# Optimization experiments

Hardware: AMD Instinct MI355X
Metric: run time of the kernel (lower is better)

The kernel has to match this reference:

```python
import jax, jax.numpy as jnp
import numpy as np

N = 50000        # nodes
E = 800000       # edges (avg degree 16)
F = 64           # in/out feature dim (scatter into zeros_like(x) forces out==in)
H = 128          # hidden dim
CIN = 2 * F + 1  # combined_features dim


def setup_inputs() -> dict:
    key = jax.random.key(0)
    ks = jax.random.split(key, 12)
    x = jax.random.normal(ks[0], (N, F), dtype=jnp.float32)
    pos = jax.random.normal(ks[1], (N, 3), dtype=jnp.float32)
    edge_index = jax.random.randint(ks[2], (2, E), 0, N, dtype=jnp.int64)
    s1 = 1.0 / np.sqrt(CIN)
    s2 = 1.0 / np.sqrt(H)
    W1x = jax.random.uniform(ks[3], (CIN, H), jnp.float32, -s1, s1)
    b1x = jax.random.uniform(ks[4], (H,), jnp.float32, -s1, s1)
    W2x = jax.random.uniform(ks[5], (H, F), jnp.float32, -s2, s2)
    b2x = jax.random.uniform(ks[6], (F,), jnp.float32, -s2, s2)
    W1p = jax.random.uniform(ks[7], (CIN, H), jnp.float32, -s1, s1)
    b1p = jax.random.uniform(ks[8], (H,), jnp.float32, -s1, s1)
    W2p = jax.random.uniform(ks[9], (H, 1), jnp.float32, -s2, s2)
    b2p = jax.random.uniform(ks[10], (1,), jnp.float32, -s2, s2)
    return {"x": x, "pos": pos, "edge_index": edge_index,
            "W1x": W1x, "b1x": b1x, "W2x": W2x, "b2x": b2x,
            "W1p": W1p, "b1p": b1p, "W2p": W2p, "b2p": b2p}


def reference(x, pos, edge_index, W1x, b1x, W2x, b2x, W1p, b1p, W2p, b2p):
    row, col = edge_index[0], edge_index[1]
    rel_pos = pos[row] - pos[col]                              # [E, 3]
    dist_sq = jnp.sum(rel_pos * rel_pos, axis=-1, keepdims=True)  # [E, 1]
    combined = jnp.concatenate([x[row], x[col], dist_sq], axis=-1)  # [E, 2F+1]
    # phi_x: Linear -> SiLU -> Linear
    msg_x = jax.nn.silu(combined @ W1x + b1x) @ W2x + b2x      # [E, F]
    aggregated_x = jax.ops.segment_sum(msg_x, col, num_segments=x.shape[0])
    # phi_pos: Linear -> SiLU -> Linear (scalar weight per edge)
    weight_pos = jax.nn.silu(combined @ W1p + b1p) @ W2p + b2p  # [E, 1]
    pos_update = weight_pos * rel_pos                           # [E, 3]
    aggregated_pos = jax.ops.segment_sum(pos_update, col, num_segments=pos.shape[0])
    return aggregated_x, aggregated_pos
```

## Files before the change

### kernel.cpp

```cpp
#include <hip/hip_runtime.h>

typedef short short8 __attribute__((ext_vector_type(8)));
typedef float floatx4 __attribute__((ext_vector_type(4)));

__device__ __forceinline__ unsigned short f2bf(float f) {
  unsigned int u = __float_as_uint(f);
  u += 0x7FFFu + ((u >> 16) & 1u);
  return (unsigned short)(u >> 16);
}

#if __has_builtin(__builtin_amdgcn_cvt_pk_bf16_f32)
typedef __bf16 bf16x2_t __attribute__((ext_vector_type(2)));
__device__ __forceinline__ unsigned int pk2bf(float lo, float hi) {
  bf16x2_t v = __builtin_amdgcn_cvt_pk_bf16_f32(lo, hi);
  return __builtin_bit_cast(unsigned int, v);
}
#else
__device__ __forceinline__ unsigned int pk2bf(float lo, float hi) {
  return (unsigned)f2bf(lo) | ((unsigned)f2bf(hi) << 16);
}
#endif

__global__ void k_xcvt(const float* __restrict__ x, unsigned short* __restrict__ xb, int n) {
  int i = (blockIdx.x * 256 + threadIdx.x) * 8;
  if (i < n) {
    float4 a = *(const float4*)(x + i);
    float4 b = *(const float4*)(x + i + 4);
    uint4 o;
    o.x = pk2bf(a.x, a.y); o.y = pk2bf(a.z, a.w);
    o.z = pk2bf(b.x, b.y); o.w = pk2bf(b.z, b.w);
    *(uint4*)(xb + i) = o;
  }
}

__global__ void prep_weights(const float* __restrict__ W1x, const float* __restrict__ W1p,
                             const float* __restrict__ b1x, const float* __restrict__ b1p,
                             const float* __restrict__ W2x, unsigned short* __restrict__ wbuf) {
  int i = blockIdx.x * 256 + threadIdx.x;
  if (i >= 49152) return;
  float v;
  if (i < 40960) {
    const float* W = (i < 20480) ? W1x : W1p;
    const float* B = (i < 20480) ? b1x : b1p;
    int j = (i < 20480) ? i : i - 20480;
    int jj   = j & 7;
    int lane = (j >> 3) & 63;
    int ks   = (j >> 9) % 5;
    int nt   = j / 2560;
    int k = ks*32 + (lane >> 4)*8 + jj;
    int n = nt*16 + (lane & 15);
    v = (k < 129) ? W[k*128 + n] : (k == 129 ? B[n] : 0.0f);
  } else {
    int j = i - 40960;
    int jj   = j & 7;
    int lane = (j >> 3) & 63;
    int ks   = (j >> 9) & 3;
    int nt   = j >> 11;
    int k = ks*32 + (lane >> 4)*8 + jj;
    int n = nt*16 + (lane & 15);
    v = W2x[k*64 + n];
  }
  wbuf[i] = f2bf(v);
}

__global__ void k_hist(const int* __restrict__ col, int E, int* __restrict__ hist) {
  int i = blockIdx.x * 256 + threadIdx.x;
  if (i < E) atomicAdd(&hist[col[i]], 1);
}

__global__ __launch_bounds__(256) void k_scan_a(const int* __restrict__ hist, int N,
                                                int* __restrict__ excl, int* __restrict__ bsum) {
  __shared__ int wtot[4], wexc[4];
  int t = threadIdx.x, lane = t & 63, w = t >> 6;
  int base = blockIdx.x * 1024 + t * 4;
  int v0 = (base + 0 < N) ? hist[base + 0] : 0;
  int v1 = (base + 1 < N) ? hist[base + 1] : 0;
  int v2 = (base + 2 < N) ? hist[base + 2] : 0;
  int v3 = (base + 3 < N) ? hist[base + 3] : 0;
  int T = v0 + v1 + v2 + v3;
  int inc = T;
  #pragma unroll
  for (int s = 1; s < 64; s <<= 1) {
    int u = __shfl_up(inc, s, 64);
    if (lane >= s) inc += u;
  }
  if (lane == 63) wtot[w] = inc;
  __syncthreads();
  if (t == 0) {
    int a = 0;
    #pragma unroll
    for (int i = 0; i < 4; ++i) { wexc[i] = a; a += wtot[i]; }
    bsum[blockIdx.x] = a;
  }
  __syncthreads();
  int tex = wexc[w] + (inc - T);
  if (base + 0 < N) excl[base + 0] = tex;
  if (base + 1 < N) excl[base + 1] = tex + v0;
  if (base + 2 < N) excl[base + 2] = tex + v0 + v1;
  if (base + 3 < N) excl[base + 3] = tex + v0 + v1 + v2;
}

__global__ void k_scan_b(const int* __restrict__ bsum, int* __restrict__ boff, int NB) {
  int lane = threadIdx.x;
  int v = (lane < NB) ? bsum[lane] : 0;
  int inc = v;
  #pragma unroll
  for (int s = 1; s < 64; s <<= 1) {
    int u = __shfl_up(inc, s, 64);
    if (lane >= s) inc += u;
  }
  if (lane < NB) boff[lane] = inc - v;
}

__global__ void k_scatter(const int* __restrict__ row, const int* __restrict__ col, int E,
                          int* __restrict__ excl, const int* __restrict__ boff,
                          int2* __restrict__ sedge) {
  int i = blockIdx.x * 256 + threadIdx.x;
  if (i < E) {
    int c = col[i];
    int p = atomicAdd(&excl[c], 1) + boff[c >> 10];
    sedge[p] = make_int2(row[i], c);
  }
}

__global__ __launch_bounds__(256) void mp_main(
    const float* __restrict__ x, const unsigned short* __restrict__ xb, int use_xb,
    const float* __restrict__ pos,
    const int2* __restrict__ sedge,
    const int* __restrict__ rowp, const int* __restrict__ colp,
    int E, int sorted,
    const float* __restrict__ b2x, const float* __restrict__ W2p,
    const float* __restrict__ b2p,
    const unsigned short* __restrict__ wbuf,
    float* __restrict__ out_x, float* __restrict__ out_pos)
{
  __shared__ __align__(16) unsigned short C_lds[64][168];
  __shared__ __align__(16) unsigned short H_lds[64][136];
  __shared__ float rel_lds[64][3];
  __shared__ int   col_sh[64];
  __shared__ float wsum[4][64];

  const int t    = threadIdx.x;
  const int e0   = blockIdx.x * 64;
  const int wv   = t >> 6;
  const int lane = t & 63;
  const int quad = lane >> 4;
  const int lc   = lane & 15;

  if (t < 64) {
    int e = e0 + t;
    float rp0 = 0.f, rp1 = 0.f, rp2 = 0.f, dsq = 0.f; int c = -1;
    if (e < E) {
      int r;
      if (sorted) { int2 rc = sedge[e]; r = rc.x; c = rc.y; }
      else        { r = rowp[e]; c = colp[e]; }
      float pr0 = pos[r*3+0], pr1 = pos[r*3+1], pr2 = pos[r*3+2];
      float pc0 = pos[c*3+0], pc1 = pos[c*3+1], pc2 = pos[c*3+2];
      rp0 = pr0 - pc0; rp1 = pr1 - pc1; rp2 = pr2 - pc2;
      dsq = rp0*rp0 + rp1*rp1 + rp2*rp2;
    }
    rel_lds[t][0] = rp0; rel_lds[t][1] = rp1; rel_lds[t][2] = rp2;
    col_sh[t] = c;
    C_lds[t][128] = f2bf(dsq);
    C_lds[t][129] = 0x3F80;
    #pragma unroll
    for (int k = 130; k < 160; ++k) C_lds[t][k] = 0;
  }
  {
    const int s = t >> 2, p = t & 3;
    const int e = e0 + s;
    uint4 r0, r1, c0, c1;
    if (e < E) {
      int r, c;
      if (sorted) { int2 rc = sedge[e]; r = rc.x; c = rc.y; }
      else        { r = rowp[e]; c = colp[e]; }
      if (use_xb) {
        const uint4* xr = (const uint4*)(xb + (size_t)r*64 + p*16);
        const uint4* xc = (const uint4*)(xb + (size_t)c*64 + p*16);
        r0 = xr[0]; r1 = xr[1];
        c0 = xc[0]; c1 = xc[1];
      } else {
        const float4* xr = (const float4*)(x + (size_t)r*64 + p*16);
        const float4* xc = (const float4*)(x + (size_t)c*64 + p*16);
        float4 a0 = xr[0], a1 = xr[1], a2 = xr[2], a3 = xr[3];
        float4 d0 = xc[0], d1 = xc[1], d2 = xc[2], d3 = xc[3];
        r0 = make_uint4(pk2bf(a0.x,a0.y), pk2bf(a0.z,a0.w), pk2bf(a1.x,a1.y), pk2bf(a1.z,a1.w));
        r1 = make_uint4(pk2bf(a2.x,a2.y), pk2bf(a2.z,a2.w), pk2bf(a3.x,a3.y), pk2bf(a3.z,a3.w));
        c0 = make_uint4(pk2bf(d0.x,d0.y), pk2bf(d0.z,d0.w), pk2bf(d1.x,d1.y), pk2bf(d1.z,d1.w));
        c1 = make_uint4(pk2bf(d2.x,d2.y), pk2bf(d2.z,d2.w), pk2bf(d3.x,d3.y), pk2bf(d3.z,d3.w));
      }
    } else {
      r0 = r1 = c0 = c1 = make_uint4(0u, 0u, 0u, 0u);
    }
    uint4* dr = (uint4*)&C_lds[s][p*16];
    dr[0] = r0; dr[1] = r1;
    uint4* dc = (uint4*)&C_lds[s][64 + p*16];
    dc[0] = c0; dc[1] = c1;
  }
  __syncthreads();

  const short8* __restrict__ w1x_f = (const short8*)(wbuf);
  const short8* __restrict__ w1p_f = (const short8*)(wbuf + 20480);
  const short8* __restrict__ w2x_f = (const short8*)(wbuf + 40960);

  short8 a1x[2][5], a1p[2][5], a2w[4];
  #pragma unroll
  for (int i = 0; i < 2; ++i) {
    int hti = wv + 4*i;
    #pragma unroll
    for (int ks = 0; ks < 5; ++ks) {
      a1x[i][ks] = w1x_f[(hti*5 + ks)*64 + lane];
      a1p[i][ks] = w1p_f[(hti*5 + ks)*64 + lane];
    }
  }
  #pragma unroll
  for (int ks = 0; ks < 4; ++ks) a2w[ks] = w2x_f[(wv*4 + ks)*64 + lane];

  float wp2[2][4], b2xr[4];
  #pragma unroll
  for (int i = 0; i < 2; ++i)
    #pragma unroll
    for (int r = 0; r < 4; ++r) wp2[i][r] = W2p[(wv + 4*i)*16 + quad*4 + r];
  #pragma unroll
  for (int r = 0; r < 4; ++r) b2xr[r] = b2x[wv*16 + quad*4 + r];
  const float b2ps = b2p[0];

  #pragma unroll 2
  for (int et = 0; et < 4; ++et) {
    floatx4 ax0 = {0,0,0,0}, ax1 = {0,0,0,0}, ap0 = {0,0,0,0}, ap1 = {0,0,0,0};
    #pragma unroll
    for (int ks = 0; ks < 5; ++ks) {
      short8 b = *(const short8*)&C_lds[et*16 + lc][ks*32 + quad*8];
      ax0 = __builtin_amdgcn_mfma_f32_16x16x32_bf16(a1x[0][ks], b, ax0, 0, 0, 0);
      ax1 = __builtin_amdgcn_mfma_f32_16x16x32_bf16(a1x[1][ks], b, ax1, 0, 0, 0);
      ap0 = __builtin_amdgcn_mfma_f32_16x16x32_bf16(a1p[0][ks], b, ap0, 0, 0, 0);
      ap1 = __builtin_amdgcn_mfma_f32_16x16x32_bf16(a1p[1][ks], b, ap1, 0, 0, 0);
    }
    float ps = 0.f;
    #pragma unroll
    for (int i = 0; i < 2; ++i) {
      floatx4 axx = i ? ax1 : ax0;
      floatx4 app = i ? ap1 : ap0;
      float sx[4];
      #pragma unroll
      for (int r = 0; r < 4; ++r) {
        float h  = axx[r];
        sx[r] = h * __builtin_amdgcn_rcpf(1.f + __expf(-h));
        float hp = app[r];
        float sp = hp * __builtin_amdgcn_rcpf(1.f + __expf(-hp));
        ps += sp * wp2[i][r];
      }
      *(uint2*)&H_lds[et*16 + lc][(wv + 4*i)*16 + quad*4] =
          make_uint2(pk2bf(sx[0], sx[1]), pk2bf(sx[2], sx[3]));
    }
    ps += __shfl_xor(ps, 16, 64);
    ps += __shfl_xor(ps, 32, 64);
    if (lane < 16) wsum[wv][et*16 + lane] = ps;
  }
  __syncthreads();

  #pragma unroll 2
  for (int et = 0; et < 4; ++et) {
    floatx4 acc = {0,0,0,0};
    #pragma unroll
    for (int ks = 0; ks < 4; ++ks) {
      short8 b = *(const short8*)&H_lds[et*16 + lc][ks*32 + quad*8];
      acc = __builtin_amdgcn_mfma_f32_16x16x32_bf16(a2w[ks], b, acc, 0, 0, 0);
    }
    int edge = et*16 + lc;
    int myc = col_sh[edge];
    float v0 = acc[0] + b2xr[0], v1 = acc[1] + b2xr[1];
    float v2 = acc[2] + b2xr[2], v3 = acc[3] + b2xr[3];
    if (sorted) {
      #pragma unroll
      for (int s = 1; s < 16; s <<= 1) {
        int   nc  = __shfl_down(myc, s, 64);
        float n0  = __shfl_down(v0,  s, 64);
        float n1  = __shfl_down(v1,  s, 64);
        float n2  = __shfl_down(v2,  s, 64);
        float n3  = __shfl_down(v3,  s, 64);
        if ((lc + s < 16) && (nc == myc)) { v0 += n0; v1 += n1; v2 += n2; v3 += n3; }
      }
    }
    bool head = (myc >= 0) && (!sorted || lc == 0 || col_sh[edge-1] != myc);
    if (head) {
      float* dst = out_x + (size_t)myc*64 + wv*16 + quad*4;
      atomicAdd(dst + 0, v0);
      atomicAdd(dst + 1, v1);
      atomicAdd(dst + 2, v2);
      atomicAdd(dst + 3, v3);
    }
  }

  if (t < 64) {
    int c = col_sh[t];
    float w = wsum[0][t] + wsum[1][t] + wsum[2][t] + wsum[3][t] + b2ps;
    float p0 = w * rel_lds[t][0], p1 = w * rel_lds[t][1], p2 = w * rel_lds[t][2];
    if (sorted) {
      #pragma unroll
      for (int s = 1; s < 64; s <<= 1) {
        int   nc = __shfl_down(c,  s, 64);
        float n0 = __shfl_down(p0, s, 64);
        float n1 = __shfl_down(p1, s, 64);
        float n2 = __shfl_down(p2, s, 64);
        if ((t + s < 64) && (nc == c)) { p0 += n0; p1 += n1; p2 += n2; }
      }
    }
    bool head = (c >= 0) && (!sorted || t == 0 || col_sh[t-1] != c);
    if (head) {
      atomicAdd(&out_pos[(size_t)c*3 + 0], p0);
      atomicAdd(&out_pos[(size_t)c*3 + 1], p1);
      atomicAdd(&out_pos[(size_t)c*3 + 2], p2);
    }
  }
}

extern "C" void kernel_launch(void* const* d_in, const int* in_sizes, int n_in,
                              void* d_out, int out_size, void* d_ws, size_t ws_size,
                              hipStream_t stream) {
  const float* x   = (const float*)d_in[0];
  const float* pos = (const float*)d_in[1];
  const int*   ei  = (const int*)d_in[2];
  const float* W1x = (const float*)d_in[3];
  const float* b1x = (const float*)d_in[4];
  const float* W2x = (const float*)d_in[5];
  const float* b2x = (const float*)d_in[6];
  const float* W1p = (const float*)d_in[7];
  const float* b1p = (const float*)d_in[8];
  const float* W2p = (const float*)d_in[9];
  const float* b2p = (const float*)d_in[10];

  const int E = in_sizes[2] / 2;
  const int N = in_sizes[0] / 64;
  const int* rowp = ei;
  const int* colp = ei + E;
  float* out_x   = (float*)d_out;
  float* out_pos = out_x + (size_t)N * 64;

  char* ws = (char*)d_ws;
  const size_t xb_bytes = (size_t)N * 64 * 2;
  size_t base = 0;
  int use_xb = 0;
  {
    size_t needA = xb_bytes + 98304 + 200192 + 512 + 512 + (size_t)E * 8;
    if (ws_size >= needA) { use_xb = 1; base = xb_bytes; }
  }
  unsigned short* xb   = (unsigned short*)ws;
  unsigned short* wbuf = (unsigned short*)(ws + base);
  int*  off   = (int*)(ws + base + 98304);
  int*  bsum  = (int*)(ws + base + 98304 + 200192);
  int*  boff  = (int*)(ws + base + 98304 + 200192 + 512);
  int2* sedge = (int2*)(ws + base + 98304 + 200192 + 1024);
  const size_t need_sort = base + 98304 + 200192 + 1024 + (size_t)E * 8;
  const int use_sort = (ws_size >= need_sort) ? 1 : 0;

  hipMemsetAsync(d_out, 0, (size_t)out_size * sizeof(float), stream);
  if (use_xb)
    k_xcvt<<<(N*64 + 2047) / 2048, 256, 0, stream>>>(x, xb, N*64);
  prep_weights<<<192, 256, 0, stream>>>(W1x, W1p, b1x, b1p, W2x, wbuf);

  if (use_sort) {
    const int NB = (N + 1023) / 1024;
    hipMemsetAsync(off, 0, (size_t)N * sizeof(int), stream);
    k_hist<<<(E + 255) / 256, 256, 0, stream>>>(colp, E, off);
    k_scan_a<<<NB, 256, 0, stream>>>(off, N, off, bsum);
    k_scan_b<<<1, 64, 0, stream>>>(bsum, boff, NB);
    k_scatter<<<(E + 255) / 256, 256, 0, stream>>>(rowp, colp, E, off, boff, sedge);
  }

  mp_main<<<(E + 63) / 64, 256, 0, stream>>>(x, xb, use_xb, pos, sedge, rowp, colp,
                                             E, use_sort, b2x, W2p, b2p,
                                             wbuf, out_x, out_pos);
}
```

Before: 348.9 us.

## Merge setup kernels, fold block scan into scatter, remap blocks per XCD, reuse LDS

Replaces two memsets plus the conversion and weight-prep kernels with one multi-role setup kernel, and folds the tiny block-offset scan into the scatter kernel. This removes several launches and their gaps. The main kernel now remaps block IDs so each group of 8 interleaved blocks handles a contiguous edge range, which should keep neighbouring sorted edges on the same XCD for L2 locality. It also hoists the weight loads before the gather, drops H_lds by reusing C_lds behind an extra barrier, and stops unrolling the first loop. Together these cut LDS use and may raise occupancy, at the cost of one more sync per iteration.

```diff
diff --git a/kernel.cpp b/kernel.cpp
--- a/kernel.cpp
+++ b/kernel.cpp
@@ -21,46 +21,63 @@
 }
 #endif
 
-__global__ void k_xcvt(const float* __restrict__ x, unsigned short* __restrict__ xb, int n) {
-  int i = (blockIdx.x * 256 + threadIdx.x) * 8;
-  if (i < n) {
-    float4 a = *(const float4*)(x + i);
-    float4 b = *(const float4*)(x + i + 4);
-    uint4 o;
-    o.x = pk2bf(a.x, a.y); o.y = pk2bf(a.z, a.w);
-    o.z = pk2bf(b.x, b.y); o.w = pk2bf(b.z, b.w);
-    *(uint4*)(xb + i) = o;
-  }
-}
-
-__global__ void prep_weights(const float* __restrict__ W1x, const float* __restrict__ W1p,
-                             const float* __restrict__ b1x, const float* __restrict__ b1p,
-                             const float* __restrict__ W2x, unsigned short* __restrict__ wbuf) {
-  int i = blockIdx.x * 256 + threadIdx.x;
-  if (i >= 49152) return;
-  float v;
-  if (i < 40960) {
-    const float* W = (i < 20480) ? W1x : W1p;
-    const float* B = (i < 20480) ? b1x : b1p;
-    int j = (i < 20480) ? i : i - 20480;
-    int jj   = j & 7;
-    int lane = (j >> 3) & 63;
-    int ks   = (j >> 9) % 5;
-    int nt   = j / 2560;
-    int k = ks*32 + (lane >> 4)*8 + jj;
-    int n = nt*16 + (lane & 15);
-    v = (k < 129) ? W[k*128 + n] : (k == 129 ? B[n] : 0.0f);
+__global__ __launch_bounds__(256) void k_setup(
+    float* __restrict__ out, int out_n,
+    int* __restrict__ hist, int N,
+    const float* __restrict__ x, unsigned short* __restrict__ xb, int nx,
+    const float* __restrict__ W1x, const float* __restrict__ W1p,
+    const float* __restrict__ b1x, const float* __restrict__ b1p,
+    const float* __restrict__ W2x, unsigned short* __restrict__ wbuf,
+    int b1, int b2, int b3)
+{
+  int blk = blockIdx.x, t = threadIdx.x;
+  if (blk < b1) {
+    int i = (blk * 256 + t) * 4;
+    if (i + 4 <= out_n) {
+      *(float4*)(out + i) = make_float4(0.f, 0.f, 0.f, 0.f);
+    } else {
+      for (int k = i; k < out_n; ++k) out[k] = 0.f;
+    }
+  } else if (blk < b2) {
+    int i = (blk - b1) * 256 + t;
+    if (i < N) hist[i] = 0;
+  } else if (blk < b3) {
+    int i = ((blk - b2) * 256 + t) * 8;
+    if (i < nx) {
+      float4 a = *(const float4*)(x + i);
+      float4 b = *(const float4*)(x + i + 4);
+      uint4 o;
+      o.x = pk2bf(a.x, a.y); o.y = pk2bf(a.z, a.w);
+      o.z = pk2bf(b.x, b.y); o.w = pk2bf(b.z, b.w);
+      *(uint4*)(xb + i) = o;
+    }
   } else {
-    int j = i - 40960;
-    int jj   = j & 7;
-    int lane = (j >> 3) & 63;
-    int ks   = (j >> 9) & 3;
-    int nt   = j >> 11;
-    int k = ks*32 + (lane >> 4)*8 + jj;
-    int n = nt*16 + (lane & 15);
-    v = W2x[k*64 + n];
-  }
-  wbuf[i] = f2bf(v);
+    int i = (blk - b3) * 256 + t;
+    if (i >= 49152) return;
+    float v;
+    if (i < 40960) {
+      const float* W = (i < 20480) ? W1x : W1p;
+      const float* B = (i < 20480) ? b1x : b1p;
+      int j = (i < 20480) ? i : i - 20480;
+      int jj   = j & 7;
+      int lane = (j >> 3) & 63;
+      int ks   = (j >> 9) % 5;
+      int nt   = j / 2560;
+      int k = ks*32 + (lane >> 4)*8 + jj;
+      int n = nt*16 + (lane & 15);
+      v = (k < 129) ? W[k*128 + n] : (k == 129 ? B[n] : 0.0f);
+    } else {
+      int j = i - 40960;
+      int jj   = j & 7;
+      int lane = (j >> 3) & 63;
+      int ks   = (j >> 9) & 3;
+      int nt   = j >> 11;
+      int k = ks*32 + (lane >> 4)*8 + jj;
+      int n = nt*16 + (lane & 15);
+      v = W2x[k*64 + n];
+    }
+    wbuf[i] = f2bf(v);
+  }
 }
 
 __global__ void k_hist(const int* __restrict__ col, int E, int* __restrict__ hist) {
@@ -100,25 +117,27 @@
   if (base + 3 < N) excl[base + 3] = tex + v0 + v1 + v2;
 }
 
-__global__ void k_scan_b(const int* __restrict__ bsum, int* __restrict__ boff, int NB) {
-  int lane = threadIdx.x;
-  int v = (lane < NB) ? bsum[lane] : 0;
-  int inc = v;
-  #pragma unroll
-  for (int s = 1; s < 64; s <<= 1) {
-    int u = __shfl_up(inc, s, 64);
-    if (lane >= s) inc += u;
-  }
-  if (lane < NB) boff[lane] = inc - v;
-}
-
-__global__ void k_scatter(const int* __restrict__ row, const int* __restrict__ col, int E,
-                          int* __restrict__ excl, const int* __restrict__ boff,
-                          int2* __restrict__ sedge) {
-  int i = blockIdx.x * 256 + threadIdx.x;
+__global__ __launch_bounds__(256) void k_scatter(
+    const int* __restrict__ row, const int* __restrict__ col, int E,
+    int* __restrict__ excl, const int* __restrict__ bsum, int NB,
+    int2* __restrict__ sedge) {
+  __shared__ int boff_sh[64];
+  int t = threadIdx.x;
+  if (t < 64) {
+    int v = (t < NB) ? bsum[t] : 0;
+    int inc = v;
+    #pragma unroll
+    for (int s = 1; s < 64; s <<= 1) {
+      int u = __shfl_up(inc, s, 64);
+      if (t >= s) inc += u;
+    }
+    boff_sh[t] = inc - v;
+  }
+  __syncthreads();
+  int i = blockIdx.x * 256 + t;
   if (i < E) {
     int c = col[i];
-    int p = atomicAdd(&excl[c], 1) + boff[c >> 10];
+    int p = atomicAdd(&excl[c], 1) + boff_sh[c >> 10];
     sedge[p] = make_int2(row[i], c);
   }
 }
@@ -128,24 +147,53 @@
     const float* __restrict__ pos,
     const int2* __restrict__ sedge,
     const int* __restrict__ rowp, const int* __restrict__ colp,
-    int E, int sorted,
+    int E, int sorted, int chunk,
     const float* __restrict__ b2x, const float* __restrict__ W2p,
     const float* __restrict__ b2p,
     const unsigned short* __restrict__ wbuf,
     float* __restrict__ out_x, float* __restrict__ out_pos)
 {
   __shared__ __align__(16) unsigned short C_lds[64][168];
-  __shared__ __align__(16) unsigned short H_lds[64][136];
   __shared__ float rel_lds[64][3];
   __shared__ int   col_sh[64];
   __shared__ float wsum[4][64];
 
+  const int nblk = (E + 63) >> 6;
+  const int logical = (blockIdx.x & 7) * chunk + (blockIdx.x >> 3);
+  if (logical >= nblk) return;
+  const int e0 = logical * 64;
+
   const int t    = threadIdx.x;
-  const int e0   = blockIdx.x * 64;
   const int wv   = t >> 6;
   const int lane = t & 63;
   const int quad = lane >> 4;
   const int lc   = lane & 15;
+
+  const short8* __restrict__ w1x_f = (const short8*)(wbuf);
+  const short8* __restrict__ w1p_f = (const short8*)(wbuf + 20480);
+  const short8* __restrict__ w2x_f = (const short8*)(wbuf + 40960);
+
+  short8 a1x[2][5], a1p[2][5], a2w[4];
+  #pragma unroll
+  for (int i = 0; i < 2; ++i) {
+    int hti = wv + 4*i;
+    #pragma unroll
+    for (int ks = 0; ks < 5; ++ks) {
+      a1x[i][ks] = w1x_f[(hti*5 + ks)*64 + lane];
+      a1p[i][ks] = w1p_f[(hti*5 + ks)*64 + lane];
+    }
+  }
+  #pragma unroll
+  for (int ks = 0; ks < 4; ++ks) a2w[ks] = w2x_f[(wv*4 + ks)*64 + lane];
+
+  float wp2[2][4], b2xr[4];
+  #pragma unroll
+  for (int i = 0; i < 2; ++i)
+    #pragma unroll
+    for (int r = 0; r < 4; ++r) wp2[i][r] = W2p[(wv + 4*i)*16 + quad*4 + r];
+  #pragma unroll
+  for (int r = 0; r < 4; ++r) b2xr[r] = b2x[wv*16 + quad*4 + r];
+  const float b2ps = b2p[0];
 
   if (t < 64) {
     int e = e0 + t;
@@ -199,33 +247,7 @@
   }
   __syncthreads();
 
-  const short8* __restrict__ w1x_f = (const short8*)(wbuf);
-  const short8* __restrict__ w1p_f = (const short8*)(wbuf + 20480);
-  const short8* __restrict__ w2x_f = (const short8*)(wbuf + 40960);
-
-  short8 a1x[2][5], a1p[2][5], a2w[4];
-  #pragma unroll
-  for (int i = 0; i < 2; ++i) {
-    int hti = wv + 4*i;
-    #pragma unroll
-    for (int ks = 0; ks < 5; ++ks) {
-      a1x[i][ks] = w1x_f[(hti*5 + ks)*64 + lane];
-      a1p[i][ks] = w1p_f[(hti*5 + ks)*64 + lane];
-    }
-  }
-  #pragma unroll
-  for (int ks = 0; ks < 4; ++ks) a2w[ks] = w2x_f[(wv*4 + ks)*64 + lane];
-
-  float wp2[2][4], b2xr[4];
-  #pragma unroll
-  for (int i = 0; i < 2; ++i)
-    #pragma unroll
-    for (int r = 0; r < 4; ++r) wp2[i][r] = W2p[(wv + 4*i)*16 + quad*4 + r];
-  #pragma unroll
-  for (int r = 0; r < 4; ++r) b2xr[r] = b2x[wv*16 + quad*4 + r];
-  const float b2ps = b2p[0];
-
-  #pragma unroll 2
+  #pragma unroll 1
   for (int et = 0; et < 4; ++et) {
     floatx4 ax0 = {0,0,0,0}, ax1 = {0,0,0,0}, ap0 = {0,0,0,0}, ap1 = {0,0,0,0};
     #pragma unroll
@@ -237,6 +259,7 @@
       ap1 = __builtin_amdgcn_mfma_f32_16x16x32_bf16(a1p[1][ks], b, ap1, 0, 0, 0);
     }
     float ps = 0.f;
+    uint2 hw[2];
     #pragma unroll
     for (int i = 0; i < 2; ++i) {
       floatx4 axx = i ? ax1 : ax0;
@@ -250,9 +273,12 @@
         float sp = hp * __builtin_amdgcn_rcpf(1.f + __expf(-hp));
         ps += sp * wp2[i][r];
       }
-      *(uint2*)&H_lds[et*16 + lc][(wv + 4*i)*16 + quad*4] =
-          make_uint2(pk2bf(sx[0], sx[1]), pk2bf(sx[2], sx[3]));
-    }
+      hw[i] = make_uint2(pk2bf(sx[0], sx[1]), pk2bf(sx[2], sx[3]));
+    }
+    __syncthreads();
+    #pragma unroll
+    for (int i = 0; i < 2; ++i)
+      *(uint2*)&C_lds[et*16 + lc][(wv + 4*i)*16 + quad*4] = hw[i];
     ps += __shfl_xor(ps, 16, 64);
     ps += __shfl_xor(ps, 32, 64);
     if (lane < 16) wsum[wv][et*16 + lane] = ps;
@@ -264,7 +290,7 @@
     floatx4 acc = {0,0,0,0};
     #pragma unroll
     for (int ks = 0; ks < 4; ++ks) {
-      short8 b = *(const short8*)&H_lds[et*16 + lc][ks*32 + quad*8];
+      short8 b = *(const short8*)&C_lds[et*16 + lc][ks*32 + quad*8];
       acc = __builtin_amdgcn_mfma_f32_16x16x32_bf16(a2w[ks], b, acc, 0, 0, 0);
     }
     int edge = et*16 + lc;
@@ -342,33 +368,38 @@
   size_t base = 0;
   int use_xb = 0;
   {
-    size_t needA = xb_bytes + 98304 + 200192 + 512 + 512 + (size_t)E * 8;
+    size_t needA = xb_bytes + 98304 + 200192 + 512 + (size_t)E * 8;
     if (ws_size >= needA) { use_xb = 1; base = xb_bytes; }
   }
   unsigned short* xb   = (unsigned short*)ws;
   unsigned short* wbuf = (unsigned short*)(ws + base);
   int*  off   = (int*)(ws + base + 98304);
   int*  bsum  = (int*)(ws + base + 98304 + 200192);
-  int*  boff  = (int*)(ws + base + 98304 + 200192 + 512);
-  int2* sedge = (int2*)(ws + base + 98304 + 200192 + 1024);
-  const size_t need_sort = base + 98304 + 200192 + 1024 + (size_t)E * 8;
+  int2* sedge = (int2*)(ws + base + 98304 + 200192 + 512);
+  const size_t need_sort = base + 98304 + 200192 + 512 + (size_t)E * 8;
   const int use_sort = (ws_size >= need_sort) ? 1 : 0;
 
-  hipMemsetAsync(d_out, 0, (size_t)out_size * sizeof(float), stream);
-  if (use_xb)
-    k_xcvt<<<(N*64 + 2047) / 2048, 256, 0, stream>>>(x, xb, N*64);
-  prep_weights<<<192, 256, 0, stream>>>(W1x, W1p, b1x, b1p, W2x, wbuf);
+  const int nx = N * 64;
+  const int nb_out  = (out_size + 1023) / 1024;
+  const int nb_hist = use_sort ? (N + 255) / 256 : 0;
+  const int nb_xcvt = use_xb ? (nx + 2047) / 2048 : 0;
+  const int nb_prep = 192;
+  const int b1 = nb_out, b2 = b1 + nb_hist, b3 = b2 + nb_xcvt;
+  const int setup_blocks = b3 + nb_prep;
+  k_setup<<<setup_blocks, 256, 0, stream>>>(
+      (float*)d_out, out_size, off, N, x, xb, nx,
+      W1x, W1p, b1x, b1p, W2x, wbuf, b1, b2, b3);
 
   if (use_sort) {
     const int NB = (N + 1023) / 1024;
-    hipMemsetAsync(off, 0, (size_t)N * sizeof(int), stream);
     k_hist<<<(E + 255) / 256, 256, 0, stream>>>(colp, E, off);
     k_scan_a<<<NB, 256, 0, stream>>>(off, N, off, bsum);
-    k_scan_b<<<1, 64, 0, stream>>>(bsum, boff, NB);
-    k_scatter<<<(E + 255) / 256, 256, 0, stream>>>(rowp, colp, E, off, boff, sedge);
-  }
-
-  mp_main<<<(E + 63) / 64, 256, 0, stream>>>(x, xb, use_xb, pos, sedge, rowp, colp,
-                                             E, use_sort, b2x, W2p, b2p,
-                                             wbuf, out_x, out_pos);
-}
+    k_scatter<<<(E + 255) / 256, 256, 0, stream>>>(rowp, colp, E, off, bsum, NB, sedge);
+  }
+
+  const int nblk  = (E + 63) / 64;
+  const int chunk = (nblk + 7) / 8;
+  mp_main<<<chunk * 8, 256, 0, stream>>>(x, xb, use_xb, pos, sedge, rowp, colp,
+                                         E, use_sort, chunk, b2x, W2p, b2p,
+                                         wbuf, out_x, out_pos);
+}
```

Result: slower. 363.5 us (+4.2%).
